# Optimization experiments

Hardware: AMD Instinct MI355X
Metric: run time of the kernel (lower is better)

Reference implementation:

```python
import jax, jax.numpy as jnp
import numpy as np

N = 8192          # tokens
D_IN = 32768      # dec_input_size (SAE latent dim)
D_OUT = 768       # dec_hidden_size (model resid dim)


def setup_inputs() -> dict:
    key = jax.random.key(0)
    kx, kw = jax.random.split(key)
    x = jax.random.normal(kx, (N, D_IN), dtype=jnp.float32)
    W = jax.random.normal(kw, (D_OUT, D_IN), dtype=jnp.float32) * (1.0 / np.sqrt(D_IN))
    b_pre = jnp.zeros((D_IN,), dtype=jnp.float32)
    return {"x": x, "W": W, "b_pre": b_pre}


def reference(x, W, b_pre):
    # x: [N, D_in]; subtract pre-bias, then dense decode: (x - b_pre) @ W^T -> [N, D_out]
    x_adj = x - b_pre
    return jnp.einsum('nd,od->no', x_adj, W)
```

## Files before the change

kernel.cpp:

```cpp
#include <hip/hip_runtime.h>
#include <hip/hip_bf16.h>

#define TOK 8192
#define OUTD 768
#define KD 32768

#define BM 128
#define BN 768
#define BK 32
#define SPLITK 4
#define KCHUNK (KD / SPLITK)
#define NKT (KCHUNK / BK)
#define NHT_TOT (KD / BK)
#define THREADS 512
#define HTILE (BN * BK * 2)
#define ATILE (BM * BK * 2)

#define WSOFF_W 4096
#define WSOFF_P (WSOFF_W + (long)NHT_TOT * HTILE)
#define PSTRIDE ((long)TOK * OUTD)

typedef __attribute__((ext_vector_type(4))) float f32x4;
typedef __attribute__((ext_vector_type(16))) float f32x16;
typedef __attribute__((ext_vector_type(8))) short bf16x8;
typedef __attribute__((ext_vector_type(4))) unsigned int u32x4;

__device__ __forceinline__ unsigned pack2(float lo, float hi) {
    __hip_bfloat162 h = __float22bfloat162_rn(make_float2(lo, hi));
    unsigned u;
    __builtin_memcpy(&u, &h, 4);
    return u;
}

__device__ __forceinline__ u32x4 cvt_chunk(f32x4 a, f32x4 b) {
    u32x4 r;
    r[0] = pack2(a[0], a[1]);
    r[1] = pack2(a[2], a[3]);
    r[2] = pack2(b[0], b[1]);
    r[3] = pack2(b[2], b[3]);
    return r;
}

__global__ void colbias_kernel(const float* __restrict__ W,
                               const float* __restrict__ bp,
                               float* __restrict__ negc) {
    int o = blockIdx.x;
    int tid = threadIdx.x;
    const float* wr = W + (long)o * KD;
    float s = 0.f;
    for (int i = tid * 4; i < KD; i += 256 * 4) {
        f32x4 w = *(const f32x4*)(wr + i);
        f32x4 b = *(const f32x4*)(bp + i);
        s += w[0] * b[0] + w[1] * b[1] + w[2] * b[2] + w[3] * b[3];
    }
    #pragma unroll
    for (int off = 32; off > 0; off >>= 1) s += __shfl_down(s, off);
    __shared__ float red[4];
    if ((tid & 63) == 0) red[tid >> 6] = s;
    __syncthreads();
    if (tid == 0) negc[o] = -(red[0] + red[1] + red[2] + red[3]);
}

__global__ void cast_w_kernel(const float* __restrict__ W,
                              char* __restrict__ wsW) {
    int kth = blockIdx.x;
    int tid = threadIdx.x;
    int q = tid & 3;
    int c0 = tid >> 2;
    #pragma unroll
    for (int i = 0; i < 6; ++i) {
        int c = c0 + i * 128;
        const float* src = W + (long)c * KD + kth * 32 + q * 8;
        f32x4 a = ((const f32x4*)src)[0];
        f32x4 b = ((const f32x4*)src)[1];
        char* dst = wsW + (long)kth * HTILE + c * 64 + ((q ^ (c & 3)) << 4);
        *(u32x4*)dst = cvt_chunk(a, b);
    }
}

__global__ __launch_bounds__(THREADS, 1) void decoder_gemm(
    const float* __restrict__ X, const char* __restrict__ Wb16,
    float* __restrict__ P) {
    __shared__ char lds[ATILE + 3 * HTILE];
    char* ldsA = lds;
    char* ldsB = lds + ATILE;

    const int bid = blockIdx.x;
    const int ks = bid & (SPLITK - 1);
    const int mt = bid >> 2;
    const int row0 = mt * BM;

    const int tid = threadIdx.x;
    const int lane = tid & 63;
    const int wid = tid >> 6;
    const int wm = wid >> 2;
    const int wn = wid & 3;
    const int l31 = lane & 31;
    const int hi = lane >> 5;

    const float* Xb = X + (long)row0 * KD + (long)ks * KCHUNK;
    const char* Wt0 = Wb16 + (long)ks * NKT * HTILE;

    const int ar = tid >> 2;
    const int aq = tid & 3;
    f32x4 xr[2];

    auto LOADA = [&](int kt) {
        const f32x4* p = (const f32x4*)(Xb + (long)ar * KD + kt * 32 + aq * 8);
        xr[0] = p[0];
        xr[1] = p[1];
    };

    const int asoff = ar * 64 + ((aq ^ (ar & 3)) << 4);

    auto STOREA = [&]() {
        *(u32x4*)(ldsA + asoff) = cvt_chunk(xr[0], xr[1]);
    };

    auto ISSUEB = [&](int kt, int buf) {
        const char* src = Wt0 + (long)kt * HTILE + tid * 16;
        char* dst = ldsB + buf * HTILE + tid * 16;
        #pragma unroll
        for (int j = 0; j < 6; ++j)
            __builtin_amdgcn_global_load_lds(
                (const __attribute__((address_space(1))) void*)(src + j * 8192),
                (__attribute__((address_space(3))) void*)(dst + j * 8192),
                16, 0, 0);
    };

    int aoff[2], boff[6];
    #pragma unroll
    for (int m = 0; m < 2; ++m) {
        int row = wm * 64 + m * 32 + l31;
        aoff[m] = row * 64 + ((hi ^ (row & 3)) << 4);
    }
    #pragma unroll
    for (int n = 0; n < 6; ++n) {
        int col = wn * 192 + n * 32 + l31;
        boff[n] = col * 64 + ((hi ^ (col & 3)) << 4);
    }

    f32x16 acc[2][6];
    #pragma unroll
    for (int m = 0; m < 2; ++m)
        #pragma unroll
        for (int n = 0; n < 6; ++n)
            #pragma unroll
            for (int r = 0; r < 16; ++r) acc[m][n][r] = 0.f;

    auto COMPUTE = [&](int bbuf) {
        const char* As = ldsA;
        const char* Bs = ldsB + bbuf * HTILE;
        #pragma unroll
        for (int kk = 0; kk < 2; ++kk) {
            bf16x8 afr[2], bfr[6];
            #pragma unroll
            for (int m = 0; m < 2; ++m)
                afr[m] = *(const bf16x8*)(As + (aoff[m] ^ (kk << 5)));
            #pragma unroll
            for (int n = 0; n < 6; ++n)
                bfr[n] = *(const bf16x8*)(Bs + (boff[n] ^ (kk << 5)));
            __builtin_amdgcn_s_setprio(1);
            #pragma unroll
            for (int m = 0; m < 2; ++m)
                #pragma unroll
                for (int n = 0; n < 6; ++n)
                    acc[m][n] = __builtin_amdgcn_mfma_f32_32x32x16_bf16(
                        afr[m], bfr[n], acc[m][n], 0, 0, 0);
            __builtin_amdgcn_s_setprio(0);
        }
    };

    LOADA(0);
    ISSUEB(0, 0);
    STOREA();
    ISSUEB(1, 1);
    asm volatile("s_waitcnt vmcnt(6) lgkmcnt(0)" ::: "memory");
    __builtin_amdgcn_sched_barrier(0);
    __builtin_amdgcn_s_barrier();

    for (int kt = 0; kt < NKT; ++kt) {
        if (kt + 1 < NKT) LOADA(kt + 1);
        if (kt + 2 < NKT) ISSUEB(kt + 2, (kt + 2) % 3);
        COMPUTE(kt % 3);
        __builtin_amdgcn_s_barrier();
        if (kt + 1 < NKT) STOREA();
        if (kt + 2 < NKT) {
            asm volatile("s_waitcnt vmcnt(6) lgkmcnt(0)" ::: "memory");
        } else {
            asm volatile("s_waitcnt vmcnt(0) lgkmcnt(0)" ::: "memory");
        }
        __builtin_amdgcn_sched_barrier(0);
        __builtin_amdgcn_s_barrier();
    }

    float* Pk = P + (long)ks * PSTRIDE;
    #pragma unroll
    for (int m = 0; m < 2; ++m) {
        int rowb = row0 + wm * 64 + m * 32 + 4 * hi;
        #pragma unroll
        for (int n = 0; n < 6; ++n) {
            int col = wn * 192 + n * 32 + l31;
            #pragma unroll
            for (int r = 0; r < 16; ++r) {
                int row = rowb + (r & 3) + 8 * (r >> 2);
                Pk[(long)row * OUTD + col] = acc[m][n][r];
            }
        }
    }
}

__global__ void reduce_kernel(const float* __restrict__ P,
                              const float* __restrict__ negc,
                              float* __restrict__ out) {
    long i4 = ((long)blockIdx.x * blockDim.x + threadIdx.x) * 4;
    int col = (int)(i4 % OUTD);
    f32x4 s = *(const f32x4*)(negc + col);
    #pragma unroll
    for (int ks = 0; ks < SPLITK; ++ks)
        s += *(const f32x4*)(P + ks * PSTRIDE + i4);
    *(f32x4*)(out + i4) = s;
}

extern "C" void kernel_launch(void* const* d_in, const int* in_sizes, int n_in,
                              void* d_out, int out_size, void* d_ws,
                              size_t ws_size, hipStream_t stream) {
    const float* x = (const float*)d_in[0];
    const float* W = (const float*)d_in[1];
    const float* bp = (const float*)d_in[2];
    float* out = (float*)d_out;
    float* negc = (float*)d_ws;
    char* wsW = (char*)d_ws + WSOFF_W;
    float* wsP = (float*)((char*)d_ws + WSOFF_P);

    hipLaunchKernelGGL(colbias_kernel, dim3(OUTD), dim3(256), 0, stream, W, bp,
                       negc);
    hipLaunchKernelGGL(cast_w_kernel, dim3(NHT_TOT), dim3(512), 0, stream, W,
                       wsW);
    hipLaunchKernelGGL(decoder_gemm, dim3((TOK / BM) * SPLITK), dim3(THREADS),
                       0, stream, x, wsW, wsP);
    hipLaunchKernelGGL(reduce_kernel, dim3((TOK * OUTD) / (256 * 4)), dim3(256),
                       0, stream, wsP, negc, out);
}
```

Before: 629.9 us.

## Give each wave private W tile buffers and double-buffer the A tile

Each of the 8 waves now computes all 128 rows against its own 96-column slice of W, loading that slice into a per-wave LDS ring with global_load_lds. Because a wave only reads B data it loaded itself, only a per-wave vmcnt wait is needed before compute. The A tile is double-buffered, so each iteration needs one block barrier instead of two, and the last two iterations are peeled out of the loop. In exchange the A fragment reads per wave double (4x3 MFMA tiles instead of 2x6), which raises LDS read traffic. LDS use and register pressure also change.

```diff
diff --git a/kernel.cpp b/kernel.cpp
--- a/kernel.cpp
+++ b/kernel.cpp
@@ -15,6 +15,7 @@
 #define THREADS 512
 #define HTILE (BN * BK * 2)
 #define ATILE (BM * BK * 2)
+#define WBUF 6144
 
 #define WSOFF_W 4096
 #define WSOFF_P (WSOFF_W + (long)NHT_TOT * HTILE)
@@ -81,9 +82,9 @@
 __global__ __launch_bounds__(THREADS, 1) void decoder_gemm(
     const float* __restrict__ X, const char* __restrict__ Wb16,
     float* __restrict__ P) {
-    __shared__ char lds[ATILE + 3 * HTILE];
+    __shared__ char lds[2 * ATILE + 24 * WBUF];
     char* ldsA = lds;
-    char* ldsB = lds + ATILE;
+    char* ldsB = lds + 2 * ATILE;
 
     const int bid = blockIdx.x;
     const int ks = bid & (SPLITK - 1);
@@ -93,13 +94,12 @@
     const int tid = threadIdx.x;
     const int lane = tid & 63;
     const int wid = tid >> 6;
-    const int wm = wid >> 2;
-    const int wn = wid & 3;
     const int l31 = lane & 31;
     const int hi = lane >> 5;
 
     const float* Xb = X + (long)row0 * KD + (long)ks * KCHUNK;
-    const char* Wt0 = Wb16 + (long)ks * NKT * HTILE;
+    const char* Wt0 = Wb16 + (long)ks * NKT * HTILE + wid * WBUF;
+    char* myB = ldsB + wid * 3 * WBUF;
 
     const int ar = tid >> 2;
     const int aq = tid & 3;
@@ -113,58 +113,58 @@
 
     const int asoff = ar * 64 + ((aq ^ (ar & 3)) << 4);
 
-    auto STOREA = [&]() {
-        *(u32x4*)(ldsA + asoff) = cvt_chunk(xr[0], xr[1]);
+    auto STOREA = [&](int buf) {
+        *(u32x4*)(ldsA + buf * ATILE + asoff) = cvt_chunk(xr[0], xr[1]);
     };
 
     auto ISSUEB = [&](int kt, int buf) {
-        const char* src = Wt0 + (long)kt * HTILE + tid * 16;
-        char* dst = ldsB + buf * HTILE + tid * 16;
+        const char* src = Wt0 + (long)kt * HTILE + lane * 16;
+        char* dst = myB + buf * WBUF + lane * 16;
         #pragma unroll
         for (int j = 0; j < 6; ++j)
             __builtin_amdgcn_global_load_lds(
-                (const __attribute__((address_space(1))) void*)(src + j * 8192),
-                (__attribute__((address_space(3))) void*)(dst + j * 8192),
+                (const __attribute__((address_space(1))) void*)(src + j * 1024),
+                (__attribute__((address_space(3))) void*)(dst + j * 1024),
                 16, 0, 0);
     };
 
-    int aoff[2], boff[6];
-    #pragma unroll
-    for (int m = 0; m < 2; ++m) {
-        int row = wm * 64 + m * 32 + l31;
+    int aoff[4], boff[3];
+    #pragma unroll
+    for (int m = 0; m < 4; ++m) {
+        int row = m * 32 + l31;
         aoff[m] = row * 64 + ((hi ^ (row & 3)) << 4);
     }
     #pragma unroll
-    for (int n = 0; n < 6; ++n) {
-        int col = wn * 192 + n * 32 + l31;
-        boff[n] = col * 64 + ((hi ^ (col & 3)) << 4);
-    }
-
-    f32x16 acc[2][6];
-    #pragma unroll
-    for (int m = 0; m < 2; ++m)
-        #pragma unroll
-        for (int n = 0; n < 6; ++n)
+    for (int n = 0; n < 3; ++n) {
+        int c = n * 32 + l31;
+        boff[n] = c * 64 + ((hi ^ (c & 3)) << 4);
+    }
+
+    f32x16 acc[4][3];
+    #pragma unroll
+    for (int m = 0; m < 4; ++m)
+        #pragma unroll
+        for (int n = 0; n < 3; ++n)
             #pragma unroll
             for (int r = 0; r < 16; ++r) acc[m][n][r] = 0.f;
 
-    auto COMPUTE = [&](int bbuf) {
-        const char* As = ldsA;
-        const char* Bs = ldsB + bbuf * HTILE;
+    auto COMPUTE = [&](int b3, int abuf) {
+        const char* As = ldsA + abuf * ATILE;
+        const char* Bs = myB + b3 * WBUF;
         #pragma unroll
         for (int kk = 0; kk < 2; ++kk) {
-            bf16x8 afr[2], bfr[6];
-            #pragma unroll
-            for (int m = 0; m < 2; ++m)
+            bf16x8 afr[4], bfr[3];
+            #pragma unroll
+            for (int n = 0; n < 3; ++n)
+                bfr[n] = *(const bf16x8*)(Bs + (boff[n] ^ (kk << 5)));
+            #pragma unroll
+            for (int m = 0; m < 4; ++m)
                 afr[m] = *(const bf16x8*)(As + (aoff[m] ^ (kk << 5)));
-            #pragma unroll
-            for (int n = 0; n < 6; ++n)
-                bfr[n] = *(const bf16x8*)(Bs + (boff[n] ^ (kk << 5)));
             __builtin_amdgcn_s_setprio(1);
             #pragma unroll
-            for (int m = 0; m < 2; ++m)
+            for (int m = 0; m < 4; ++m)
                 #pragma unroll
-                for (int n = 0; n < 6; ++n)
+                for (int n = 0; n < 3; ++n)
                     acc[m][n] = __builtin_amdgcn_mfma_f32_32x32x16_bf16(
                         afr[m], bfr[n], acc[m][n], 0, 0, 0);
             __builtin_amdgcn_s_setprio(0);
@@ -173,34 +173,42 @@
 
     LOADA(0);
     ISSUEB(0, 0);
-    STOREA();
+    STOREA(0);
     ISSUEB(1, 1);
     asm volatile("s_waitcnt vmcnt(6) lgkmcnt(0)" ::: "memory");
     __builtin_amdgcn_sched_barrier(0);
     __builtin_amdgcn_s_barrier();
 
-    for (int kt = 0; kt < NKT; ++kt) {
-        if (kt + 1 < NKT) LOADA(kt + 1);
-        if (kt + 2 < NKT) ISSUEB(kt + 2, (kt + 2) % 3);
-        COMPUTE(kt % 3);
-        __builtin_amdgcn_s_barrier();
-        if (kt + 1 < NKT) STOREA();
-        if (kt + 2 < NKT) {
-            asm volatile("s_waitcnt vmcnt(6) lgkmcnt(0)" ::: "memory");
-        } else {
-            asm volatile("s_waitcnt vmcnt(0) lgkmcnt(0)" ::: "memory");
-        }
+    for (int kt = 0; kt < NKT - 2; ++kt) {
+        LOADA(kt + 1);
+        ISSUEB(kt + 2, (kt + 2) % 3);
+        asm volatile("s_waitcnt vmcnt(8)" ::: "memory");
+        __builtin_amdgcn_sched_barrier(0);
+        COMPUTE(kt % 3, kt & 1);
+        STOREA((kt + 1) & 1);
+        asm volatile("s_waitcnt lgkmcnt(0)" ::: "memory");
         __builtin_amdgcn_sched_barrier(0);
         __builtin_amdgcn_s_barrier();
     }
 
+    LOADA(NKT - 1);
+    asm volatile("s_waitcnt vmcnt(2)" ::: "memory");
+    __builtin_amdgcn_sched_barrier(0);
+    COMPUTE((NKT - 2) % 3, (NKT - 2) & 1);
+    STOREA((NKT - 1) & 1);
+    asm volatile("s_waitcnt lgkmcnt(0)" ::: "memory");
+    __builtin_amdgcn_sched_barrier(0);
+    __builtin_amdgcn_s_barrier();
+
+    COMPUTE((NKT - 1) % 3, (NKT - 1) & 1);
+
     float* Pk = P + (long)ks * PSTRIDE;
     #pragma unroll
-    for (int m = 0; m < 2; ++m) {
-        int rowb = row0 + wm * 64 + m * 32 + 4 * hi;
-        #pragma unroll
-        for (int n = 0; n < 6; ++n) {
-            int col = wn * 192 + n * 32 + l31;
+    for (int m = 0; m < 4; ++m) {
+        int rowb = row0 + m * 32 + 4 * hi;
+        #pragma unroll
+        for (int n = 0; n < 3; ++n) {
+            int col = wid * 96 + n * 32 + l31;
             #pragma unroll
             for (int r = 0; r < 16; ++r) {
                 int row = rowb + (r & 3) + 8 * (r >> 2);
```

Result: slower. 644.4 us (+2.3%).
